# Kernel optimization log

Measured on AMD Instinct MI355X. Metric: run time of the kernel, lower is better.

## Reference

```python
import jax, jax.numpy as jnp
import numpy as np

N_DST = 100_000
N_SRC = 200_000
DEG = 16            # fixed avg degree -> E = N_DST*DEG
E = N_DST * DEG
P, K, W = 16, 256, 8  # num_parts, codebook entries, part width; feat_dim = P*W = 128
F_IN = P * W
F_OUT = 128


def setup_inputs() -> dict:
    key = jax.random.key(0)
    k1, k2, k3, k4, k5, k6, k7 = jax.random.split(key, 7)
    codes = jax.random.randint(k1, (N_SRC, P), 0, K, dtype=jnp.int32)
    indices = jax.random.randint(k2, (E,), 0, N_SRC, dtype=jnp.int32)
    indptr = (jnp.arange(N_DST + 1, dtype=jnp.int32) * DEG)
    h_self = jax.random.normal(k3, (N_DST, F_IN), dtype=jnp.float32)
    codebook = jax.random.normal(k4, (P, K, W), dtype=jnp.float32)
    W_neigh = jax.random.normal(k5, (F_OUT, F_IN), dtype=jnp.float32) * (1.0 / np.sqrt(F_IN))
    W_self = jax.random.normal(k6, (F_OUT, F_IN), dtype=jnp.float32) * (1.0 / np.sqrt(F_IN))
    b_self = jax.random.normal(k7, (F_OUT,), dtype=jnp.float32) * 0.01
    return {"codes": codes, "indices": indices, "indptr": indptr, "h_self": h_self,
            "codebook": codebook, "W_neigh": W_neigh, "W_self": W_self, "b_self": b_self}


def reference(codes, indices, indptr, h_self, codebook, W_neigh, W_self, b_self):
    n_dst = indptr.shape[0] - 1
    n_edges = indices.shape[0]
    # --- VQ decompress: codebook[p, codes[n, p]] -> [N_src, P, W] -> [N_src, F_IN]
    feat = codebook[jnp.arange(P)[None, :], codes]          # [N_src, P, W]
    feat = feat.reshape(feat.shape[0], F_IN)                # [N_src, F_IN]
    # --- CSR(CSC) mean SpMM over neighbors
    # dst id of each edge from indptr (jit-safe, static E)
    dst_ids = jnp.searchsorted(indptr, jnp.arange(n_edges, dtype=indptr.dtype), side="right") - 1
    gathered = feat[indices]                                 # [E, F_IN] (irregular gather)
    summed = jax.ops.segment_sum(gathered, dst_ids, num_segments=n_dst)  # [N_dst, F_IN]
    deg = jnp.diff(indptr).astype(summed.dtype)
    h_neigh = summed / jnp.maximum(deg, 1.0)[:, None]        # mean aggregation
    # --- linear combine: fc_neigh(h_neigh) + fc_self(h_self)
    rst = h_neigh @ W_neigh.T + h_self @ W_self.T + b_self[None, :]
    return rst
```

## Files before the change

### kernel.cpp

```cpp
#include <hip/hip_runtime.h>
#include <stdint.h>

constexpr int N_DST = 100000;
constexpr int N_SRC = 200000;
constexpr int DEG   = 16;
constexpr int PP    = 16;
constexpr int KK    = 256;
constexpr int WW    = 8;
constexpr int F_IN  = 128;
constexpr int F_OUT = 128;
constexpr int NSTRIPE = N_DST / 16;

typedef __attribute__((ext_vector_type(8))) short short8;
typedef __attribute__((ext_vector_type(4))) float floatx4;

__device__ __forceinline__ unsigned short f2bf(float f) {
    unsigned int u = __float_as_uint(f);
    unsigned int r = (u + 0x7FFFu + ((u >> 16) & 1u)) >> 16;
    return (unsigned short)r;
}
__device__ __forceinline__ float bf_lo(unsigned int q) {
    return __uint_as_float(q << 16);
}
__device__ __forceinline__ float bf_hi(unsigned int q) {
    return __uint_as_float(q & 0xFFFF0000u);
}


__global__ __launch_bounds__(256) void pack_codes(
    const int* __restrict__ codes, unsigned int* __restrict__ pc32)
{
    constexpr int N32 = N_SRC * PP / 4;
    for (int i = blockIdx.x * 256 + threadIdx.x; i < N32; i += gridDim.x * 256) {
        const int4 v = ((const int4*)codes)[i];
        pc32[i] = (unsigned int)(v.x & 255) | ((unsigned int)(v.y & 255) << 8)
                | ((unsigned int)(v.z & 255) << 16) | ((unsigned int)(v.w & 255) << 24);
    }
}

template <bool PACKED>
__global__ __launch_bounds__(512, 2) void fused_kernel(
    const int* __restrict__ codes, const unsigned char* __restrict__ pcodes,
    const int* __restrict__ indices,
    const float* __restrict__ codebook, const float* __restrict__ h_self,
    const float* __restrict__ Wn, const float* __restrict__ Ws,
    const float* __restrict__ b_self, float* __restrict__ out)
{
    __shared__ __align__(16) unsigned short scb[KK * PP * WW];
    __shared__ __align__(16) unsigned short wlds[F_OUT][256];
    __shared__ __align__(16) unsigned short tbuf[8][16][128];

    const int tid  = threadIdx.x;
    const int wv   = tid >> 6;
    const int lane = tid & 63;
    const int quad = lane >> 4;
    const int r    = lane & 15;
    const int p    = lane & 15;
    const int sub  = lane >> 4;

    {
        const float4* cb4 = (const float4*)codebook;
        ushort4* s4 = (ushort4*)scb;
        #pragma unroll
        for (int it = 0; it < 16; ++it) {
            const int i = tid + it * 512;
            const float4 v = cb4[i];
            const int pp_  = i >> 9;
            const int k    = (i >> 1) & 255;
            const int half = i & 1;
            ushort4 w;
            w.x = f2bf(v.x); w.y = f2bf(v.y); w.z = f2bf(v.z); w.w = f2bf(v.w);
            s4[((k << 4) | pp_) * 2 + half] = w;
        }
    }

    #pragma unroll
    for (int j = 0; j < 16; ++j) {
        const int fi = tid + j * 512;
        const int o  = fi >> 6;
        const int fc = fi & 63;
        const int k  = fc * 4;
        const float* src = (k < 128) ? (Wn + o * 128 + k)
                                     : (Ws + o * 128 + (k - 128));
        const float4 v = *(const float4*)src;
        ushort4 w;
        w.x = f2bf(v.x); w.y = f2bf(v.y); w.z = f2bf(v.z); w.w = f2bf(v.w);
        const int ch = fc >> 1;
        const int hc = fc & 1;
        *(ushort4*)&wlds[o][((ch ^ (o & 7)) << 3) + hc * 4] = w;
    }

    float bsv[8];
    #pragma unroll
    for (int cg = 0; cg < 8; ++cg) bsv[cg] = b_self[cg * 16 + r];

    __syncthreads();

    auto do_unit = [&](const int* cc, int u) {
        float ga[8];
        #pragma unroll
        for (int i = 0; i < 8; ++i) ga[i] = 0.f;
        #pragma unroll
        for (int e = 0; e < 16; ++e) {
            const uint4 q = *(const uint4*)(scb + (((cc[e] << 4) | p) << 3));
            ga[0] += bf_lo(q.x); ga[1] += bf_hi(q.x);
            ga[2] += bf_lo(q.y); ga[3] += bf_hi(q.y);
            ga[4] += bf_lo(q.z); ga[5] += bf_hi(q.z);
            ga[6] += bf_lo(q.w); ga[7] += bf_hi(q.w);
        }
        const int ridx = u * 4 + sub;
        uint4 o4;
        o4.x = (unsigned int)f2bf(ga[0] * 0.0625f) | ((unsigned int)f2bf(ga[1] * 0.0625f) << 16);
        o4.y = (unsigned int)f2bf(ga[2] * 0.0625f) | ((unsigned int)f2bf(ga[3] * 0.0625f) << 16);
        o4.z = (unsigned int)f2bf(ga[4] * 0.0625f) | ((unsigned int)f2bf(ga[5] * 0.0625f) << 16);
        o4.w = (unsigned int)f2bf(ga[6] * 0.0625f) | ((unsigned int)f2bf(ga[7] * 0.0625f) << 16);
        *(uint4*)&tbuf[wv][ridx][(p ^ (ridx & 7)) << 3] = o4;
    };

    auto load_srcs = [&](int S0, int u, int* sa) {
        const int* base = indices + (size_t)(S0 + u * 4 + sub) * DEG;
        #pragma unroll
        for (int j = 0; j < 4; ++j) {
            const int4 t = ((const int4*)base)[j];
            sa[j * 4 + 0] = t.x; sa[j * 4 + 1] = t.y;
            sa[j * 4 + 2] = t.z; sa[j * 4 + 3] = t.w;
        }
    };
    auto issue_pcodes = [&](const int* sa, int* cc) {
        #pragma unroll
        for (int e = 0; e < 16; ++e)
            cc[e] = pcodes[(size_t)sa[e] * PP + p];
    };
    auto issue_codes_shfl = [&](int sidx, int* cc) {
        #pragma unroll
        for (int e = 0; e < 16; ++e) {
            const int s = __shfl(sidx, (lane & 48) | e, 64);
            cc[e] = codes[s * PP + p];
        }
    };

    for (int s = blockIdx.x * 8 + wv; s < NSTRIPE; s += gridDim.x * 8) {
        const int S0 = s * 16;

        float4 hsv[8];
        #pragma unroll
        for (int k2 = 0; k2 < 4; ++k2) {
            const float* hp = h_self + (size_t)(S0 + r) * F_IN + k2 * 32 + quad * 8;
            hsv[k2 * 2]     = *(const float4*)hp;
            hsv[k2 * 2 + 1] = *(const float4*)(hp + 4);
        }

        int c0[16], c1[16], c2[16], c3[16];
        if constexpr (PACKED) {
            int sa0[16], sa1[16];
            load_srcs(S0, 0, sa0);
            load_srcs(S0, 1, sa1);
            __builtin_amdgcn_sched_barrier(0);
            issue_pcodes(sa0, c0);
            issue_pcodes(sa1, c1);
            __builtin_amdgcn_sched_barrier(0);
            int sa2[16], sa3[16];
            load_srcs(S0, 2, sa2);
            load_srcs(S0, 3, sa3);
            do_unit(c0, 0);
            issue_pcodes(sa2, c2);
            __builtin_amdgcn_sched_barrier(0);
            do_unit(c1, 1);
            issue_pcodes(sa3, c3);
            __builtin_amdgcn_sched_barrier(0);
            do_unit(c2, 2);
            do_unit(c3, 3);
        } else {
            const int sidx0 = indices[(S0     ) * DEG + lane];
            const int sidx1 = indices[(S0 +  4) * DEG + lane];
            const int sidx2 = indices[(S0 +  8) * DEG + lane];
            const int sidx3 = indices[(S0 + 12) * DEG + lane];
            __builtin_amdgcn_sched_barrier(0);
            issue_codes_shfl(sidx0, c0);
            issue_codes_shfl(sidx1, c1);
            __builtin_amdgcn_sched_barrier(0);
            do_unit(c0, 0);
            issue_codes_shfl(sidx2, c2);
            __builtin_amdgcn_sched_barrier(0);
            do_unit(c1, 1);
            issue_codes_shfl(sidx3, c3);
            __builtin_amdgcn_sched_barrier(0);
            do_unit(c2, 2);
            do_unit(c3, 3);
        }

        short8 af4[4];
        #pragma unroll
        for (int k2 = 0; k2 < 4; ++k2) {
            union { short8 v; unsigned short u[8]; } f;
            f.u[0] = f2bf(hsv[k2 * 2].x);     f.u[1] = f2bf(hsv[k2 * 2].y);
            f.u[2] = f2bf(hsv[k2 * 2].z);     f.u[3] = f2bf(hsv[k2 * 2].w);
            f.u[4] = f2bf(hsv[k2 * 2 + 1].x); f.u[5] = f2bf(hsv[k2 * 2 + 1].y);
            f.u[6] = f2bf(hsv[k2 * 2 + 1].z); f.u[7] = f2bf(hsv[k2 * 2 + 1].w);
            af4[k2] = f.v;
        }

        floatx4 acc[8];
        #pragma unroll
        for (int cg = 0; cg < 8; ++cg) acc[cg] = (floatx4)(0.f);
        #pragma unroll
        for (int kt = 0; kt < 8; ++kt) {
            short8 a;
            if (kt < 4) {
                a = *(const short8*)&tbuf[wv][r][((4 * kt + quad) ^ (r & 7)) << 3];
            } else {
                a = af4[kt - 4];
            }
            #pragma unroll
            for (int cg = 0; cg < 8; ++cg) {
                const int o = cg * 16 + r;
                const short8 b = *(const short8*)
                    &wlds[o][(((kt * 4 + quad) ^ (o & 7)) << 3)];
                acc[cg] = __builtin_amdgcn_mfma_f32_16x16x32_bf16(a, b, acc[cg], 0, 0, 0);
            }
        }

        #pragma unroll
        for (int cg = 0; cg < 8; ++cg) {
            #pragma unroll
            for (int e = 0; e < 4; ++e) {
                const int d = S0 + quad * 4 + e;
                out[(size_t)d * F_OUT + cg * 16 + r] = acc[cg][e] + bsv[cg];
            }
        }
    }
}

extern "C" void kernel_launch(void* const* d_in, const int* in_sizes, int n_in,
                              void* d_out, int out_size, void* d_ws, size_t ws_size,
                              hipStream_t stream) {
    const int*   codes    = (const int*)d_in[0];
    const int*   indices  = (const int*)d_in[1];
    const float* h_self   = (const float*)d_in[3];
    const float* codebook = (const float*)d_in[4];
    const float* W_neigh  = (const float*)d_in[5];
    const float* W_self   = (const float*)d_in[6];
    const float* b_self   = (const float*)d_in[7];
    float*       out      = (float*)d_out;

    const size_t need = (size_t)N_SRC * PP;
    if (d_ws != nullptr && ws_size >= need) {
        unsigned char* pc = (unsigned char*)d_ws;
        pack_codes<<<1024, 256, 0, stream>>>(codes, (unsigned int*)pc);
        fused_kernel<true><<<256, 512, 0, stream>>>(codes, pc, indices, codebook,
                                                    h_self, W_neigh, W_self, b_self, out);
    } else {
        fused_kernel<false><<<256, 512, 0, stream>>>(codes, nullptr, indices, codebook,
                                                     h_self, W_neigh, W_self, b_self, out);
    }
}
```

Before: 156.0 us.

## Move weights out of LDS to pre-packed bf16 global buffer, use 16-wave blocks

Adds a pack_w kernel that converts the neighbour and self weights to bf16 once per call into workspace. The packed path then reads MFMA B operands straight from global memory (L1/L2 cached) instead of staging them in LDS. The LDS this frees lets each block run 16 waves (1024 threads) with a larger tbuf, aiming for more latency hiding on the irregular code gathers. The cost is one extra kernel launch and B operand loads that now go through the vector memory path instead of LDS.

```diff
diff --git a/kernel.cpp b/kernel.cpp
--- a/kernel.cpp
+++ b/kernel.cpp
@@ -38,17 +38,26 @@
     }
 }
 
-template <bool PACKED>
-__global__ __launch_bounds__(512, 2) void fused_kernel(
-    const int* __restrict__ codes, const unsigned char* __restrict__ pcodes,
-    const int* __restrict__ indices,
+__global__ __launch_bounds__(256) void pack_w(
+    const float* __restrict__ Wn, const float* __restrict__ Ws,
+    unsigned short* __restrict__ wbf)
+{
+    const int i = blockIdx.x * 256 + threadIdx.x;
+    if (i < F_OUT * 256) {
+        const int o = i >> 8, k = i & 255;
+        const float v = (k < 128) ? Wn[o * 128 + k] : Ws[o * 128 + (k - 128)];
+        wbf[i] = f2bf(v);
+    }
+}
+
+__global__ __launch_bounds__(1024, 4) void fused16(
+    const unsigned char* __restrict__ pcodes, const int* __restrict__ indices,
     const float* __restrict__ codebook, const float* __restrict__ h_self,
-    const float* __restrict__ Wn, const float* __restrict__ Ws,
+    const unsigned short* __restrict__ wbf,
     const float* __restrict__ b_self, float* __restrict__ out)
 {
     __shared__ __align__(16) unsigned short scb[KK * PP * WW];
-    __shared__ __align__(16) unsigned short wlds[F_OUT][256];
-    __shared__ __align__(16) unsigned short tbuf[8][16][128];
+    __shared__ __align__(16) unsigned short tbuf[16][16][128];
 
     const int tid  = threadIdx.x;
     const int wv   = tid >> 6;
@@ -62,8 +71,8 @@
         const float4* cb4 = (const float4*)codebook;
         ushort4* s4 = (ushort4*)scb;
         #pragma unroll
-        for (int it = 0; it < 16; ++it) {
-            const int i = tid + it * 512;
+        for (int it = 0; it < 8; ++it) {
+            const int i = tid + it * 1024;
             const float4 v = cb4[i];
             const int pp_  = i >> 9;
             const int k    = (i >> 1) & 255;
@@ -74,27 +83,13 @@
         }
     }
 
-    #pragma unroll
-    for (int j = 0; j < 16; ++j) {
-        const int fi = tid + j * 512;
-        const int o  = fi >> 6;
-        const int fc = fi & 63;
-        const int k  = fc * 4;
-        const float* src = (k < 128) ? (Wn + o * 128 + k)
-                                     : (Ws + o * 128 + (k - 128));
-        const float4 v = *(const float4*)src;
-        ushort4 w;
-        w.x = f2bf(v.x); w.y = f2bf(v.y); w.z = f2bf(v.z); w.w = f2bf(v.w);
-        const int ch = fc >> 1;
-        const int hc = fc & 1;
-        *(ushort4*)&wlds[o][((ch ^ (o & 7)) << 3) + hc * 4] = w;
-    }
-
     float bsv[8];
     #pragma unroll
     for (int cg = 0; cg < 8; ++cg) bsv[cg] = b_self[cg * 16 + r];
 
     __syncthreads();
+
+    const unsigned short* wrow = wbf + (size_t)r * 256 + quad * 8;
 
     auto do_unit = [&](const int* cc, int u) {
         float ga[8];
@@ -116,7 +111,6 @@
         o4.w = (unsigned int)f2bf(ga[6] * 0.0625f) | ((unsigned int)f2bf(ga[7] * 0.0625f) << 16);
         *(uint4*)&tbuf[wv][ridx][(p ^ (ridx & 7)) << 3] = o4;
     };
-
     auto load_srcs = [&](int S0, int u, int* sa) {
         const int* base = indices + (size_t)(S0 + u * 4 + sub) * DEG;
         #pragma unroll
@@ -131,15 +125,8 @@
         for (int e = 0; e < 16; ++e)
             cc[e] = pcodes[(size_t)sa[e] * PP + p];
     };
-    auto issue_codes_shfl = [&](int sidx, int* cc) {
-        #pragma unroll
-        for (int e = 0; e < 16; ++e) {
-            const int s = __shfl(sidx, (lane & 48) | e, 64);
-            cc[e] = codes[s * PP + p];
-        }
-    };
-
-    for (int s = blockIdx.x * 8 + wv; s < NSTRIPE; s += gridDim.x * 8) {
+
+    for (int s = blockIdx.x * 16 + wv; s < NSTRIPE; s += gridDim.x * 16) {
         const int S0 = s * 16;
 
         float4 hsv[8];
@@ -151,7 +138,7 @@
         }
 
         int c0[16], c1[16], c2[16], c3[16];
-        if constexpr (PACKED) {
+        {
             int sa0[16], sa1[16];
             load_srcs(S0, 0, sa0);
             load_srcs(S0, 1, sa1);
@@ -170,23 +157,6 @@
             __builtin_amdgcn_sched_barrier(0);
             do_unit(c2, 2);
             do_unit(c3, 3);
-        } else {
-            const int sidx0 = indices[(S0     ) * DEG + lane];
-            const int sidx1 = indices[(S0 +  4) * DEG + lane];
-            const int sidx2 = indices[(S0 +  8) * DEG + lane];
-            const int sidx3 = indices[(S0 + 12) * DEG + lane];
-            __builtin_amdgcn_sched_barrier(0);
-            issue_codes_shfl(sidx0, c0);
-            issue_codes_shfl(sidx1, c1);
-            __builtin_amdgcn_sched_barrier(0);
-            do_unit(c0, 0);
-            issue_codes_shfl(sidx2, c2);
-            __builtin_amdgcn_sched_barrier(0);
-            do_unit(c1, 1);
-            issue_codes_shfl(sidx3, c3);
-            __builtin_amdgcn_sched_barrier(0);
-            do_unit(c2, 2);
-            do_unit(c3, 3);
         }
 
         short8 af4[4];
@@ -213,13 +183,156 @@
             }
             #pragma unroll
             for (int cg = 0; cg < 8; ++cg) {
+                const short8 b = *(const short8*)(wrow + cg * 16 * 256 + kt * 32);
+                acc[cg] = __builtin_amdgcn_mfma_f32_16x16x32_bf16(a, b, acc[cg], 0, 0, 0);
+            }
+        }
+
+        #pragma unroll
+        for (int cg = 0; cg < 8; ++cg) {
+            #pragma unroll
+            for (int e = 0; e < 4; ++e) {
+                const int d = S0 + quad * 4 + e;
+                out[(size_t)d * F_OUT + cg * 16 + r] = acc[cg][e] + bsv[cg];
+            }
+        }
+    }
+}
+
+__global__ __launch_bounds__(512, 2) void fused8(
+    const int* __restrict__ codes, const int* __restrict__ indices,
+    const float* __restrict__ codebook, const float* __restrict__ h_self,
+    const float* __restrict__ Wn, const float* __restrict__ Ws,
+    const float* __restrict__ b_self, float* __restrict__ out)
+{
+    __shared__ __align__(16) unsigned short scb[KK * PP * WW];
+    __shared__ __align__(16) unsigned short wlds[F_OUT][256];
+    __shared__ __align__(16) unsigned short tbuf[8][16][128];
+
+    const int tid  = threadIdx.x;
+    const int wv   = tid >> 6;
+    const int lane = tid & 63;
+    const int quad = lane >> 4;
+    const int r    = lane & 15;
+    const int p    = lane & 15;
+    const int sub  = lane >> 4;
+
+    {
+        const float4* cb4 = (const float4*)codebook;
+        ushort4* s4 = (ushort4*)scb;
+        #pragma unroll
+        for (int it = 0; it < 16; ++it) {
+            const int i = tid + it * 512;
+            const float4 v = cb4[i];
+            const int pp_  = i >> 9;
+            const int k    = (i >> 1) & 255;
+            const int half = i & 1;
+            ushort4 w;
+            w.x = f2bf(v.x); w.y = f2bf(v.y); w.z = f2bf(v.z); w.w = f2bf(v.w);
+            s4[((k << 4) | pp_) * 2 + half] = w;
+        }
+    }
+    #pragma unroll
+    for (int j = 0; j < 16; ++j) {
+        const int fi = tid + j * 512;
+        const int o  = fi >> 6;
+        const int fc = fi & 63;
+        const int k  = fc * 4;
+        const float* src = (k < 128) ? (Wn + o * 128 + k)
+                                     : (Ws + o * 128 + (k - 128));
+        const float4 v = *(const float4*)src;
+        ushort4 w;
+        w.x = f2bf(v.x); w.y = f2bf(v.y); w.z = f2bf(v.z); w.w = f2bf(v.w);
+        const int ch = fc >> 1;
+        const int hc = fc & 1;
+        *(ushort4*)&wlds[o][((ch ^ (o & 7)) << 3) + hc * 4] = w;
+    }
+    float bsv[8];
+    #pragma unroll
+    for (int cg = 0; cg < 8; ++cg) bsv[cg] = b_self[cg * 16 + r];
+    __syncthreads();
+
+    auto do_unit = [&](const int* cc, int u) {
+        float ga[8];
+        #pragma unroll
+        for (int i = 0; i < 8; ++i) ga[i] = 0.f;
+        #pragma unroll
+        for (int e = 0; e < 16; ++e) {
+            const uint4 q = *(const uint4*)(scb + (((cc[e] << 4) | p) << 3));
+            ga[0] += bf_lo(q.x); ga[1] += bf_hi(q.x);
+            ga[2] += bf_lo(q.y); ga[3] += bf_hi(q.y);
+            ga[4] += bf_lo(q.z); ga[5] += bf_hi(q.z);
+            ga[6] += bf_lo(q.w); ga[7] += bf_hi(q.w);
+        }
+        const int ridx = u * 4 + sub;
+        uint4 o4;
+        o4.x = (unsigned int)f2bf(ga[0] * 0.0625f) | ((unsigned int)f2bf(ga[1] * 0.0625f) << 16);
+        o4.y = (unsigned int)f2bf(ga[2] * 0.0625f) | ((unsigned int)f2bf(ga[3] * 0.0625f) << 16);
+        o4.z = (unsigned int)f2bf(ga[4] * 0.0625f) | ((unsigned int)f2bf(ga[5] * 0.0625f) << 16);
+        o4.w = (unsigned int)f2bf(ga[6] * 0.0625f) | ((unsigned int)f2bf(ga[7] * 0.0625f) << 16);
+        *(uint4*)&tbuf[wv][ridx][(p ^ (ridx & 7)) << 3] = o4;
+    };
+    auto issue_codes_shfl = [&](int sidx, int* cc) {
+        #pragma unroll
+        for (int e = 0; e < 16; ++e) {
+            const int s = __shfl(sidx, (lane & 48) | e, 64);
+            cc[e] = codes[s * PP + p];
+        }
+    };
+
+    for (int s = blockIdx.x * 8 + wv; s < NSTRIPE; s += gridDim.x * 8) {
+        const int S0 = s * 16;
+        float4 hsv[8];
+        #pragma unroll
+        for (int k2 = 0; k2 < 4; ++k2) {
+            const float* hp = h_self + (size_t)(S0 + r) * F_IN + k2 * 32 + quad * 8;
+            hsv[k2 * 2]     = *(const float4*)hp;
+            hsv[k2 * 2 + 1] = *(const float4*)(hp + 4);
+        }
+        const int sidx0 = indices[(S0     ) * DEG + lane];
+        const int sidx1 = indices[(S0 +  4) * DEG + lane];
+        const int sidx2 = indices[(S0 +  8) * DEG + lane];
+        const int sidx3 = indices[(S0 + 12) * DEG + lane];
+        __builtin_amdgcn_sched_barrier(0);
+        int c0[16], c1[16], c2[16], c3[16];
+        issue_codes_shfl(sidx0, c0);
+        issue_codes_shfl(sidx1, c1);
+        __builtin_amdgcn_sched_barrier(0);
+        do_unit(c0, 0);
+        issue_codes_shfl(sidx2, c2);
+        __builtin_amdgcn_sched_barrier(0);
+        do_unit(c1, 1);
+        issue_codes_shfl(sidx3, c3);
+        __builtin_amdgcn_sched_barrier(0);
+        do_unit(c2, 2);
+        do_unit(c3, 3);
+
+        short8 af4[4];
+        #pragma unroll
+        for (int k2 = 0; k2 < 4; ++k2) {
+            union { short8 v; unsigned short u[8]; } f;
+            f.u[0] = f2bf(hsv[k2 * 2].x);     f.u[1] = f2bf(hsv[k2 * 2].y);
+            f.u[2] = f2bf(hsv[k2 * 2].z);     f.u[3] = f2bf(hsv[k2 * 2].w);
+            f.u[4] = f2bf(hsv[k2 * 2 + 1].x); f.u[5] = f2bf(hsv[k2 * 2 + 1].y);
+            f.u[6] = f2bf(hsv[k2 * 2 + 1].z); f.u[7] = f2bf(hsv[k2 * 2 + 1].w);
+            af4[k2] = f.v;
+        }
+        floatx4 acc[8];
+        #pragma unroll
+        for (int cg = 0; cg < 8; ++cg) acc[cg] = (floatx4)(0.f);
+        #pragma unroll
+        for (int kt = 0; kt < 8; ++kt) {
+            short8 a;
+            if (kt < 4) a = *(const short8*)&tbuf[wv][r][((4 * kt + quad) ^ (r & 7)) << 3];
+            else        a = af4[kt - 4];
+            #pragma unroll
+            for (int cg = 0; cg < 8; ++cg) {
                 const int o = cg * 16 + r;
                 const short8 b = *(const short8*)
                     &wlds[o][(((kt * 4 + quad) ^ (o & 7)) << 3)];
                 acc[cg] = __builtin_amdgcn_mfma_f32_16x16x32_bf16(a, b, acc[cg], 0, 0, 0);
             }
         }
-
         #pragma unroll
         for (int cg = 0; cg < 8; ++cg) {
             #pragma unroll
@@ -243,14 +356,18 @@
     const float* b_self   = (const float*)d_in[7];
     float*       out      = (float*)d_out;
 
-    const size_t need = (size_t)N_SRC * PP;
+    const size_t pc_bytes = (size_t)N_SRC * PP;
+    const size_t woff     = (pc_bytes + 4095) & ~(size_t)4095;
+    const size_t need     = woff + (size_t)F_OUT * 256 * 2;
     if (d_ws != nullptr && ws_size >= need) {
-        unsigned char* pc = (unsigned char*)d_ws;
+        unsigned char*  pc  = (unsigned char*)d_ws;
+        unsigned short* wbf = (unsigned short*)((char*)d_ws + woff);
         pack_codes<<<1024, 256, 0, stream>>>(codes, (unsigned int*)pc);
-        fused_kernel<true><<<256, 512, 0, stream>>>(codes, pc, indices, codebook,
-                                                    h_self, W_neigh, W_self, b_self, out);
+        pack_w<<<128, 256, 0, stream>>>(W_neigh, W_self, wbf);
+        fused16<<<256, 1024, 0, stream>>>(pc, indices, codebook, h_self,
+                                          wbf, b_self, out);
     } else {
-        fused_kernel<false><<<256, 512, 0, stream>>>(codes, nullptr, indices, codebook,
-                                                     h_self, W_neigh, W_self, b_self, out);
-    }
-}
+        fused8<<<256, 512, 0, stream>>>(codes, indices, codebook, h_self,
+                                        W_neigh, W_self, b_self, out);
+    }
+}
```

After: 335.6 us. +115.1%, slower.
